# Performance work log

Hardware: AMD Instinct MI355X
Metric: run time of the kernel (lower is better)

The kernel has to match this reference:

```python
import jax, jax.numpy as jnp
import numpy as np

B, N, L = 128, 128, 128
HID = 128          # GRU hidden_size == context_dim (GRU output feeds GAT directly)
CD = 128           # context_dim
HEADS = 4
EPS = 1e-6
NEG_SLOPE = 0.2    # DenseGATConv default negative_slope


def setup_inputs() -> dict:
    key = jax.random.key(0)
    ks = jax.random.split(key, 9)
    s = 0.1
    return {
        "x": jax.random.normal(ks[0], (B, N, L, 2), jnp.float32),
        # GRU params (torch layout: weight_ih [3H, in], gate order r,z,n)
        "gru_wih": jax.random.normal(ks[1], (3 * HID, 2), jnp.float32) * s,
        "gru_whh": jax.random.normal(ks[2], (3 * HID, HID), jnp.float32) * s,
        "gru_bih": jax.random.normal(ks[3], (3 * HID,), jnp.float32) * s,
        "gru_bhh": jax.random.normal(ks[4], (3 * HID,), jnp.float32) * s,
        # DenseGATConv params: lin [heads*out, in], att_src/att_dst [heads, out], bias [out]
        "gat_w": jax.random.normal(ks[5], (HEADS * CD, CD), jnp.float32) * s,
        "gat_att_src": jax.random.normal(ks[6], (HEADS, CD), jnp.float32) * s,
        "gat_att_dst": jax.random.normal(ks[7], (HEADS, CD), jnp.float32) * s,
        "gat_bias": jnp.zeros((CD,), jnp.float32),
    }


def _forward(x, gru_wih, gru_whh, gru_bih, gru_bhh,
             gat_w, gat_att_src, gat_att_dst, gat_bias):
    b, n, l, _ = x.shape
    # --- velocity / angle feature pipeline ---
    diff = x[:, :, 1:, :] - x[:, :, :-1, :]                 # [B,N,L-1,2]
    v = jnp.sqrt(jnp.sum(diff * diff, axis=-1))             # [B,N,L-1] speeds (>=0)
    pv = jnp.concatenate([v[:, :, :1], v[:, :, :-1]], axis=2)  # previous-step speed
    cos = (pv * v) / ((jnp.abs(pv) + EPS) * (jnp.abs(v) + EPS))
    ang = jnp.arccos(jnp.clip(cos, -1.0, 1.0))
    feat = jnp.stack([v, ang], axis=-1).reshape(b * n, l - 1, 2)  # [BN,T,2]

    # --- single-layer GRU (batch_first), keep only final hidden ---
    gx = jnp.einsum('btf,gf->btg', feat, gru_wih) + gru_bih      # [BN,T,3H]
    gx = jnp.moveaxis(gx, 1, 0)                                  # [T,BN,3H]
    h0 = jnp.zeros((b * n, HID), feat.dtype)

    def step(h, g):
        gh = h @ gru_whh.T + gru_bhh
        r = jax.nn.sigmoid(g[:, :HID] + gh[:, :HID])
        z = jax.nn.sigmoid(g[:, HID:2 * HID] + gh[:, HID:2 * HID])
        nn_ = jnp.tanh(g[:, 2 * HID:] + r * gh[:, 2 * HID:])
        return (1.0 - z) * nn_ + z * h, None

    h, _ = jax.lax.scan(step, h0, gx)
    xh = h.reshape(b, n, HID)                                    # [B,N,CD]

    # --- DenseGATConv (heads=4, concat=False), adj = all ones ---
    xl = jnp.einsum('bnf,hcf->bnhc', xh, gat_w.reshape(HEADS, CD, CD))  # [B,N,H,C]
    a_src = jnp.einsum('bnhc,hc->bnh', xl, gat_att_src)
    a_dst = jnp.einsum('bnhc,hc->bnh', xl, gat_att_dst)
    alpha = a_src[:, None, :, :] + a_dst[:, :, None, :]          # [B,i,j,H]
    alpha = jax.nn.leaky_relu(alpha, NEG_SLOPE)
    alpha = jax.nn.softmax(alpha, axis=2)                        # softmax over neighbors j
    out = jnp.einsum('bijh,bjhc->bihc', alpha, xl)               # [B,N,H,C]
    out = jnp.mean(out, axis=2) + gat_bias                       # concat=False -> head mean
    return out[:, 0, :]                                          # [B,CD]


def reference(x, gru_wih, gru_whh, gru_bih, gru_bhh,
              gat_w, gat_att_src, gat_att_dst, gat_bias):
    return _forward(x, gru_wih, gru_whh, gru_bih, gru_bhh,
                    gat_w, gat_att_src, gat_att_dst, gat_bias)
```

## Files before the change

kernel.cpp:

```cpp
#include <hip/hip_runtime.h>


#define BN_TOT 16384
#define TSTEPS 127
#define LOG2E  1.44269504f

#ifndef __has_builtin
#define __has_builtin(x) 0
#endif
#if __has_builtin(__builtin_amdgcn_exp2f)
#define EXP2F(x) __builtin_amdgcn_exp2f(x)
#else
#define EXP2F(x) exp2f(x)
#endif
#if __has_builtin(__builtin_amdgcn_sqrtf)
#define FSQRT(x) __builtin_amdgcn_sqrtf(x)
#else
#define FSQRT(x) sqrtf(x)
#endif

typedef _Float16 f16x8 __attribute__((ext_vector_type(8)));
typedef float    f32x4 __attribute__((ext_vector_type(4)));

__device__ __forceinline__ float acos01(float x) {
    float s = FSQRT(1.0f - x);
    float p = fmaf(x, -0.0187293f, 0.0742610f);
    p = fmaf(x, p, -0.2121144f);
    p = fmaf(x, p, 1.5707288f);
    return s * p;
}

__global__ __launch_bounds__(256, 2) void gru_kernel(
    const float* __restrict__ x,
    const float* __restrict__ wih,
    const float* __restrict__ whh,
    const float* __restrict__ bih,
    const float* __restrict__ bhh,
    float* __restrict__ xh)
{
    __shared__ __align__(16) _Float16 h_l[2][16 * 128];
    __shared__ __align__(16) float    fstrip[4][32];

    const int tid  = threadIdx.x;
    const int wv   = tid >> 6;
    const int lane = tid & 63;
    const int c0   = lane & 15;
    const int rg   = lane >> 4;
    const int rbase = blockIdx.x * 16;

    f16x8 wr[2][4], wz[2][4], wn[2][4];
    float w0r[2], w1r[2], bbr[2], w0z[2], w1z[2], bbz[2];
    float w0n[2], w1n[2], bin_[2], bhn_[2];
    #pragma unroll
    for (int ct = 0; ct < 2; ++ct) {
        const int gr = wv * 32 + ct * 16 + c0;
        const int gz = gr + 128;
        const int gn = gr + 256;
        #pragma unroll
        for (int kt = 0; kt < 4; ++kt) {
            int ko = kt * 32 + rg * 8;
            f32x4 r0 = *(const f32x4*)&whh[gr * 128 + ko];
            f32x4 r1 = *(const f32x4*)&whh[gr * 128 + ko + 4];
            f32x4 z0 = *(const f32x4*)&whh[gz * 128 + ko];
            f32x4 z1 = *(const f32x4*)&whh[gz * 128 + ko + 4];
            f32x4 n0 = *(const f32x4*)&whh[gn * 128 + ko];
            f32x4 n1 = *(const f32x4*)&whh[gn * 128 + ko + 4];
            f16x8 fr, fz, fn;
            #pragma unroll
            for (int j = 0; j < 4; ++j) {
                fr[j]     = (_Float16)(r0[j] * LOG2E);
                fr[j + 4] = (_Float16)(r1[j] * LOG2E);
                fz[j]     = (_Float16)(z0[j] * LOG2E);
                fz[j + 4] = (_Float16)(z1[j] * LOG2E);
                fn[j]     = (_Float16)(n0[j] * (2.f * LOG2E));
                fn[j + 4] = (_Float16)(n1[j] * (2.f * LOG2E));
            }
            wr[ct][kt] = fr; wz[ct][kt] = fz; wn[ct][kt] = fn;
        }
        w0r[ct] = wih[gr * 2] * LOG2E;        w1r[ct] = wih[gr * 2 + 1] * LOG2E;
        w0z[ct] = wih[gz * 2] * LOG2E;        w1z[ct] = wih[gz * 2 + 1] * LOG2E;
        w0n[ct] = wih[gn * 2] * 2.f * LOG2E;  w1n[ct] = wih[gn * 2 + 1] * 2.f * LOG2E;
        bbr[ct] = (bih[gr] + bhh[gr]) * LOG2E;
        bbz[ct] = (bih[gz] + bhh[gz]) * LOG2E;
        bin_[ct] = bih[gn] * 2.f * LOG2E;
        bhn_[ct] = bhh[gn] * 2.f * LOG2E;
    }

    {
        int* hz = (int*)h_l[0];
        #pragma unroll
        for (int i = 0; i < 4; ++i) hz[i * 256 + tid] = 0;
    }
    __syncthreads();

    const float2* xp = (const float2*)x;
    const int r0i = rbase + c0;
    float2 xc = xp[r0i * 128 + 0];
    float2 xn = xp[r0i * 128 + 1];
    float vprev = 0.f;

    float h_reg[2][4];
    #pragma unroll
    for (int ct = 0; ct < 2; ++ct)
        #pragma unroll
        for (int i = 0; i < 4; ++i) h_reg[ct][i] = 0.f;

    const int swz_a = (c0 & 7) << 3;

    #pragma unroll 1
    for (int t = 0; t < TSTEPS; ++t) {
        {
            float dx = xn.x - xc.x, dy = xn.y - xc.y;
            float v  = FSQRT(fmaf(dx, dx, dy * dy));
            float pv = (t == 0) ? v : vprev;
            float num = pv * v;
            float den = (pv + 1e-6f) * (v + 1e-6f);
            float cs  = fminf(num * __builtin_amdgcn_rcpf(den), 1.0f);
            float an  = acos01(cs);
            vprev = v; xc = xn;
            if (t < TSTEPS - 1) xn = xp[r0i * 128 + t + 2];
            if (lane < 16)
                *(float2*)&fstrip[wv][c0 * 2] = make_float2(v, an);
        }

        const _Float16* hb = h_l[t & 1];
        _Float16*       hw = h_l[(t & 1) ^ 1];

        f32x4 f0 = *(const f32x4*)&fstrip[wv][rg * 8];
        f32x4 f1 = *(const f32x4*)&fstrip[wv][rg * 8 + 4];
        float vv[4] = {f0[0], f0[2], f1[0], f1[2]};
        float aa[4] = {f0[1], f0[3], f1[1], f1[3]};

        f16x8 afr[4];
        #pragma unroll
        for (int kt = 0; kt < 4; ++kt) {
            int ko = kt * 32 + rg * 8;
            afr[kt] = *(const f16x8*)&hb[c0 * 128 + (ko ^ swz_a)];
        }

        #pragma unroll
        for (int ct = 0; ct < 2; ++ct) {
            f32x4 ar, az, an_;
            float gxn[4];
            #pragma unroll
            for (int i = 0; i < 4; ++i) {
                ar[i]  = fmaf(vv[i], w0r[ct], fmaf(aa[i], w1r[ct], bbr[ct]));
                az[i]  = fmaf(vv[i], w0z[ct], fmaf(aa[i], w1z[ct], bbz[ct]));
                an_[i] = bhn_[ct];
                gxn[i] = fmaf(vv[i], w0n[ct], fmaf(aa[i], w1n[ct], bin_[ct]));
            }
            #pragma unroll
            for (int kt = 0; kt < 4; ++kt) {
                ar  = __builtin_amdgcn_mfma_f32_16x16x32_f16(afr[kt], wr[ct][kt], ar,  0, 0, 0);
                az  = __builtin_amdgcn_mfma_f32_16x16x32_f16(afr[kt], wz[ct][kt], az,  0, 0, 0);
                an_ = __builtin_amdgcn_mfma_f32_16x16x32_f16(afr[kt], wn[ct][kt], an_, 0, 0, 0);
            }
            #pragma unroll
            for (int i = 0; i < 4; ++i) {
                float r  = __builtin_amdgcn_rcpf(1.f + EXP2F(-ar[i]));
                float z  = __builtin_amdgcn_rcpf(1.f + EXP2F(-az[i]));
                float sn = fmaf(r, an_[i], gxn[i]);
                float nn = fmaf(-2.f, __builtin_amdgcn_rcpf(1.f + EXP2F(sn)), 1.f);
                float hv = h_reg[ct][i];
                hv = fmaf(z, hv - nn, nn);
                h_reg[ct][i] = hv;
                int row = rg * 4 + i;
                int col = wv * 32 + ct * 16 + c0;
                hw[row * 128 + (col ^ ((row & 7) << 3))] = (_Float16)hv;
            }
        }
        __syncthreads();
    }

    #pragma unroll
    for (int ct = 0; ct < 2; ++ct)
        #pragma unroll
        for (int i = 0; i < 4; ++i) {
            int r = rbase + rg * 4 + i;
            xh[r * 128 + wv * 32 + ct * 16 + c0] = h_reg[ct][i];
        }
}

__global__ __launch_bounds__(256) void gat_kernel(
    const float* __restrict__ xh,
    const float* __restrict__ gat_w,
    const float* __restrict__ att_src,
    const float* __restrict__ att_dst,
    const float* __restrict__ gbias,
    float* __restrict__ out)
{
    __shared__ __align__(16) float wse_l[512];
    __shared__ __align__(16) float wde_l[512];
    __shared__ float asrc[512];
    __shared__ float wgt[512];
    __shared__ __align__(16) float m_l[512];
    __shared__ float asd[4];

    const int b = blockIdx.x, tid = threadIdx.x;
    const float* xb = xh + b * 16384;

    #pragma unroll
    for (int p2 = 0; p2 < 2; ++p2) {
        int p = p2 * 256 + tid;
        int h = p >> 7, f = p & 127;
        float ss = 0.f, dd = 0.f;
        for (int c = 0; c < 128; ++c) {
            float w = gat_w[(h * 128 + c) * 128 + f];
            ss = fmaf(att_src[h * 128 + c], w, ss);
            dd = fmaf(att_dst[h * 128 + c], w, dd);
        }
        wse_l[p] = ss;
        wde_l[p] = dd;
    }
    __syncthreads();

    #pragma unroll
    for (int p2 = 0; p2 < 2; ++p2) {
        int p = p2 * 256 + tid;
        int j = p >> 2, h = p & 3;
        const float* wrp = wse_l + h * 128;
        const float* xr  = xb + j * 128;
        float acc = 0.f;
        for (int f = 0; f < 128; f += 4) {
            f32x4 xv  = *(const f32x4*)&xr[f];
            f32x4 wvv = *(const f32x4*)&wrp[f];
            acc += xv[0] * wvv[0] + xv[1] * wvv[1] + xv[2] * wvv[2] + xv[3] * wvv[3];
        }
        asrc[j * 4 + h] = acc;
    }
    if (tid < 4) {
        const float* wrp = wde_l + tid * 128;
        float acc = 0.f;
        for (int f = 0; f < 128; f += 4) {
            f32x4 xv  = *(const f32x4*)&xb[f];
            f32x4 wvv = *(const f32x4*)&wrp[f];
            acc += xv[0] * wvv[0] + xv[1] * wvv[1] + xv[2] * wvv[2] + xv[3] * wvv[3];
        }
        asd[tid] = acc;
    }
    __syncthreads();

    {
        int h = tid >> 6, j = tid & 63;
        float a0 = asrc[j * 4 + h] + asd[h];
        float a1 = asrc[(j + 64) * 4 + h] + asd[h];
        float e0 = a0 > 0.f ? a0 : 0.2f * a0;
        float e1 = a1 > 0.f ? a1 : 0.2f * a1;
        float mx = fmaxf(e0, e1);
        #pragma unroll
        for (int m = 32; m >= 1; m >>= 1) mx = fmaxf(mx, __shfl_xor(mx, m, 64));
        float p0 = __expf(e0 - mx), p1 = __expf(e1 - mx);
        float s = p0 + p1;
        #pragma unroll
        for (int m = 32; m >= 1; m >>= 1) s += __shfl_xor(s, m, 64);
        float inv = 1.f / s;
        wgt[j * 4 + h] = p0 * inv;
        wgt[(j + 64) * 4 + h] = p1 * inv;
    }
    __syncthreads();

    #pragma unroll
    for (int p2 = 0; p2 < 2; ++p2) {
        int p = p2 * 256 + tid;
        int h = p >> 7, f = p & 127;
        float acc = 0.f;
        for (int j = 0; j < 128; ++j)
            acc = fmaf(wgt[j * 4 + h], xb[j * 128 + f], acc);
        m_l[h * 128 + f] = acc;
    }
    __syncthreads();

    if (tid < 128) {
        int c = tid;
        float acc = 0.f;
        #pragma unroll
        for (int h = 0; h < 4; ++h) {
            const float* wrp = gat_w + (h * 128 + c) * 128;
            const float* mr  = m_l + h * 128;
            for (int f = 0; f < 128; f += 4) {
                f32x4 wvv = *(const f32x4*)&wrp[f];
                f32x4 mv  = *(const f32x4*)&mr[f];
                acc += wvv[0] * mv[0] + wvv[1] * mv[1] + wvv[2] * mv[2] + wvv[3] * mv[3];
            }
        }
        out[b * 128 + c] = 0.25f * acc + gbias[c];
    }
}

extern "C" void kernel_launch(void* const* d_in, const int* in_sizes, int n_in,
                              void* d_out, int out_size, void* d_ws, size_t ws_size,
                              hipStream_t stream) {
    const float* x       = (const float*)d_in[0];
    const float* wih     = (const float*)d_in[1];
    const float* whh     = (const float*)d_in[2];
    const float* bih     = (const float*)d_in[3];
    const float* bhh     = (const float*)d_in[4];
    const float* gat_w   = (const float*)d_in[5];
    const float* att_src = (const float*)d_in[6];
    const float* att_dst = (const float*)d_in[7];
    const float* gbias   = (const float*)d_in[8];
    float* outp = (float*)d_out;

    float* xh = (float*)d_ws;

    gru_kernel<<<1024, 256, 0, stream>>>(x, wih, whh, bih, bhh, xh);
    gat_kernel<<<128, 256, 0, stream>>>(xh, gat_w, att_src, att_dst, gbias, outp);
}
```

Measured before the change: 420.4 us.

## Precompute speed/angle features for all timesteps into LDS before GRU loop

Moves the per-step velocity/angle feature computation out of the sequential GRU recurrence. All 16 rows × 127 steps are loaded cooperatively by the whole block, turned into speeds, then angles, and stored in a 16 KB LDS table that each step reads. This removes the per-step global load latency and the scalar sqrt/acos work from the serial critical path. The cost is extra LDS, which may affect occupancy at 2 blocks per CU, plus a prologue with two barriers.

```diff
diff --git a/kernel.cpp b/kernel.cpp
--- a/kernel.cpp
+++ b/kernel.cpp
@@ -39,7 +39,7 @@
     float* __restrict__ xh)
 {
     __shared__ __align__(16) _Float16 h_l[2][16 * 128];
-    __shared__ __align__(16) float    fstrip[4][32];
+    __shared__ __align__(16) float2   f_lds[128][16];
 
     const int tid  = threadIdx.x;
     const int wv   = tid >> 6;
@@ -86,6 +86,18 @@
         bhn_[ct] = bhh[gn] * 2.f * LOG2E;
     }
 
+    const float2* xp = (const float2*)x;
+    #pragma unroll
+    for (int i = 0; i < 8; ++i) {
+        int p = i * 256 + tid;
+        int row = p >> 7, t = p & 127;
+        if (t < TSTEPS) {
+            float2 a = xp[(rbase + row) * 128 + t];
+            float2 b = xp[(rbase + row) * 128 + t + 1];
+            float dx = b.x - a.x, dy = b.y - a.y;
+            f_lds[t][row].x = FSQRT(fmaf(dx, dx, dy * dy));
+        }
+    }
     {
         int* hz = (int*)h_l[0];
         #pragma unroll
@@ -93,41 +105,37 @@
     }
     __syncthreads();
 
-    const float2* xp = (const float2*)x;
-    const int r0i = rbase + c0;
-    float2 xc = xp[r0i * 128 + 0];
-    float2 xn = xp[r0i * 128 + 1];
-    float vprev = 0.f;
-
-    float h_reg[2][4];
-    #pragma unroll
-    for (int ct = 0; ct < 2; ++ct)
-        #pragma unroll
-        for (int i = 0; i < 4; ++i) h_reg[ct][i] = 0.f;
-
-    const int swz_a = (c0 & 7) << 3;
-
-    #pragma unroll 1
-    for (int t = 0; t < TSTEPS; ++t) {
-        {
-            float dx = xn.x - xc.x, dy = xn.y - xc.y;
-            float v  = FSQRT(fmaf(dx, dx, dy * dy));
-            float pv = (t == 0) ? v : vprev;
+    #pragma unroll
+    for (int i = 0; i < 8; ++i) {
+        int p = i * 256 + tid;
+        int row = p >> 7, t = p & 127;
+        if (t < TSTEPS) {
+            float v  = f_lds[t][row].x;
+            float pv = f_lds[(t == 0) ? 0 : (t - 1)][row].x;
             float num = pv * v;
             float den = (pv + 1e-6f) * (v + 1e-6f);
             float cs  = fminf(num * __builtin_amdgcn_rcpf(den), 1.0f);
-            float an  = acos01(cs);
-            vprev = v; xc = xn;
-            if (t < TSTEPS - 1) xn = xp[r0i * 128 + t + 2];
-            if (lane < 16)
-                *(float2*)&fstrip[wv][c0 * 2] = make_float2(v, an);
-        }
-
+            f_lds[t][row].y = acos01(cs);
+        }
+    }
+    __syncthreads();
+
+    float h_reg[2][4];
+    #pragma unroll
+    for (int ct = 0; ct < 2; ++ct)
+        #pragma unroll
+        for (int i = 0; i < 4; ++i) h_reg[ct][i] = 0.f;
+
+    const int swz_a = (c0 & 7) << 3;
+
+    #pragma unroll 1
+    for (int t = 0; t < TSTEPS; ++t) {
         const _Float16* hb = h_l[t & 1];
         _Float16*       hw = h_l[(t & 1) ^ 1];
 
-        f32x4 f0 = *(const f32x4*)&fstrip[wv][rg * 8];
-        f32x4 f1 = *(const f32x4*)&fstrip[wv][rg * 8 + 4];
+        const f32x4* fb = (const f32x4*)&f_lds[t][rg * 4];
+        f32x4 f0 = fb[0];
+        f32x4 f1 = fb[1];
         float vv[4] = {f0[0], f0[2], f1[0], f1[2]};
         float aa[4] = {f0[1], f0[3], f1[1], f1[3]};
 
```

New measurement: 408.1 us. 1.03x faster.
